# Kernel tuning notes

Hardware: AMD Instinct MI355X
Metric: run time of the kernel (lower is better)

Reference implementation:

```python
import jax, jax.numpy as jnp
import numpy as np

N_NODES = 50000
E_DIM = 128
H_DIM = 256
OUT_DIM = 2
N_EDGES = 800000
NEG_SLOPE = 0.01  # nn.LeakyReLU default


def gcn_conv(x, W, b, src, dst, n):
    """PyG GCNConv: h = x @ W; add self-loops; sym-normalized scatter-add; + bias."""
    h = x @ W  # [N, H]
    loop = jnp.arange(n, dtype=src.dtype)
    s = jnp.concatenate([src, loop])
    d = jnp.concatenate([dst, loop])
    w = jnp.ones_like(s, dtype=h.dtype)
    deg = jax.ops.segment_sum(w, d, num_segments=n)  # in-degree incl. self-loop
    dis = jnp.where(deg > 0, jax.lax.rsqrt(deg), jnp.zeros_like(deg))
    norm = dis[s] * dis[d]  # [E+N]
    msg = h[s] * norm[:, None]  # gather + scale
    out = jax.ops.segment_sum(msg, d, num_segments=n)  # scatter-add to targets
    return out + b


def setup_inputs() -> dict:
    key = jax.random.key(0)
    ks = jax.random.split(key, 12)
    inp = {
        "mask_feature": jax.random.normal(ks[0], (N_NODES, E_DIM), jnp.float32),
        "feature": jax.random.normal(ks[1], (N_NODES, E_DIM), jnp.float32),
        "edge_index": jax.random.randint(ks[2], (2, N_EDGES), 0, N_NODES, jnp.int64 if jax.config.jax_enable_x64 else jnp.int32),
        "edge_type": jax.random.randint(ks[3], (N_EDGES,), 0, 2, jnp.int64 if jax.config.jax_enable_x64 else jnp.int32),
        # learned parameters
        "W_in": jax.random.normal(ks[4], (E_DIM, H_DIM), jnp.float32) * 0.05,
        "b_in": jnp.zeros((H_DIM,), jnp.float32),
        "Wg1": jax.random.normal(ks[5], (H_DIM, H_DIM), jnp.float32) * 0.05,
        "bg1": jnp.zeros((H_DIM,), jnp.float32),
        "Wg2": jax.random.normal(ks[6], (H_DIM, H_DIM), jnp.float32) * 0.05,
        "bg2": jnp.zeros((H_DIM,), jnp.float32),
        "W_out": jax.random.normal(ks[7], (H_DIM, OUT_DIM), jnp.float32) * 0.05,
        "b_out": jnp.zeros((OUT_DIM,), jnp.float32),
    }
    return inp


def reference(mask_feature, feature, edge_index, edge_type,
              W_in, b_in, Wg1, bg1, Wg2, bg2, W_out, b_out):
    src, dst = edge_index[0], edge_index[1]
    n = mask_feature.shape[0]
    # main branch
    x = jax.nn.leaky_relu(mask_feature @ W_in + b_in, NEG_SLOPE)
    x = gcn_conv(x, Wg1, bg1, src, dst, n)
    # dropout is identity at inference
    x = gcn_conv(x, Wg2, bg2, src, dst, n)
    x = x @ W_out + b_out  # [N, out_dim]
    # mask branch
    m = jax.nn.leaky_relu((feature - mask_feature) @ W_in + b_in, NEG_SLOPE)
    m = m @ W_out + b_out  # [N, out_dim]
    return x * m
```

## Files before the change

### kernel.cpp

```cpp
#include <hip/hip_runtime.h>


#define NEG_SLOPE 0.01f
constexpr int HD = 256;
constexpr int CHUNK = 4096;
constexpr int BSTRIDE = 8192;

typedef __bf16 bf16x8 __attribute__((ext_vector_type(8)));
typedef unsigned short u16x8 __attribute__((ext_vector_type(8)));
typedef float f32x4 __attribute__((ext_vector_type(4)));

#define MFMA16 __builtin_amdgcn_mfma_f32_16x16x32_bf16

__device__ inline void split1(float v, unsigned short& h, unsigned short& l) {
  unsigned u = __float_as_uint(v);
  unsigned hb = u & 0xFFFF0000u;
  float lf = v - __uint_as_float(hb);
  unsigned ul = __float_as_uint(lf);
  h = (unsigned short)(hb >> 16);
  l = (unsigned short)((ul + 0x7FFFu + ((ul >> 16) & 1u)) >> 16);
}

__global__ __launch_bounds__(256) void k_prep(
    const float* __restrict__ Win, u16x8* __restrict__ Wf,
    const float* __restrict__ Wg1, const float* __restrict__ Wg2,
    const float* __restrict__ Wo, const float* __restrict__ bg1,
    const float* __restrict__ bg2, const float* __restrict__ bo,
    float* __restrict__ wb, float* __restrict__ uv, int* __restrict__ cur) {
  __shared__ float wt[256][2];
  const int bid = blockIdx.x, tid = threadIdx.x;
  if (bid < 32) {
    int f = bid * 4 + (tid >> 6);
    int lane = tid & 63;
    int nt = f >> 3, ks = (f >> 1) & 3, hl = f & 1;
    int n = nt * 16 + (lane & 15);
    int k0 = ks * 32 + (lane >> 4) * 8;
    u16x8 outv;
    #pragma unroll
    for (int j = 0; j < 8; ++j) {
      unsigned short h, l;
      split1(Win[(size_t)(k0 + j) * HD + n], h, l);
      outv[j] = hl ? l : h;
    }
    Wf[f * 64 + lane] = outv;
  } else if (bid == 32) {
    int r = tid;
    float s0 = 0.f, s1 = 0.f;
    for (int k = 0; k < 256; ++k) {
      float w = Wg2[r * 256 + k];
      s0 = fmaf(w, Wo[k * 2 + 0], s0);
      s1 = fmaf(w, Wo[k * 2 + 1], s1);
    }
    wt[r][0] = s0; wt[r][1] = s1;
    __syncthreads();
    float b0 = 0.f, b1 = 0.f;
    for (int k = 0; k < 256; ++k) {
      float w = Wg1[r * 256 + k];
      b0 = fmaf(w, wt[k][0], b0);
      b1 = fmaf(w, wt[k][1], b1);
    }
    wb[r * 2 + 0] = b0; wb[r * 2 + 1] = b1;
    if (r < 2) {
      float u = 0.f, v = 0.f;
      for (int k = 0; k < 256; ++k) {
        u = fmaf(bg1[k], wt[k][r], u);
        v = fmaf(bg2[k], Wo[k * 2 + r], v);
      }
      uv[r] = u;
      uv[2 + r] = v + bo[r];
    }
  } else {
    cur[tid] = 0;
  }
}

__global__ __launch_bounds__(256) void k_scatter(
    const int* __restrict__ src, const int* __restrict__ dst,
    int* __restrict__ cur, unsigned* __restrict__ packed, int E) {
  __shared__ int bins[256], lstart[256], gbase[256], lcur[256];
  __shared__ int wsum[4];
  __shared__ unsigned sbuf[CHUNK];
  const int t = threadIdx.x, b = blockIdx.x;
  const int lane = t & 63, wid = t >> 6;
  bins[t] = 0;
  __syncthreads();
  const int e0 = b * CHUNK, e1 = min(e0 + CHUNK, E), m = e1 - e0;
  for (int e = e0 + t; e < e1; e += 256)
    atomicAdd(&bins[dst[e] >> 8], 1);
  __syncthreads();
  {
    int v = bins[t], incl = v;
    #pragma unroll
    for (int o = 1; o < 64; o <<= 1) {
      int tmp = __shfl_up(incl, o, 64);
      if (lane >= o) incl += tmp;
    }
    if (lane == 63) wsum[wid] = incl;
    __syncthreads();
    int woff = 0;
    for (int w = 0; w < wid; ++w) woff += wsum[w];
    int st = woff + incl - v;
    lstart[t] = st;
    lcur[t] = st;
    gbase[t] = v ? atomicAdd(&cur[t], v) : 0;
  }
  __syncthreads();
  for (int e = e0 + t; e < e1; e += 256) {
    int d = dst[e], s = src[e];
    int slot = atomicAdd(&lcur[d >> 8], 1);
    sbuf[slot] = ((unsigned)d << 16) | (unsigned)s;
  }
  __syncthreads();
  for (int i = t; i < m; i += 256) {
    unsigned pv = sbuf[i];
    int bin = pv >> 24;
    packed[(size_t)bin * BSTRIDE + gbase[bin] + (i - lstart[bin])] = pv;
  }
}

__global__ __launch_bounds__(256, 2) void k_main(
    const float* __restrict__ mf, const float* __restrict__ fe,
    const u16x8* __restrict__ Wf, const float* __restrict__ bi,
    const float* __restrict__ wb, const float* __restrict__ Wo,
    const float* __restrict__ bo, float4* __restrict__ q, float* __restrict__ Pm,
    const unsigned* __restrict__ packed, const int* __restrict__ cur,
    int* __restrict__ rp, int* __restrict__ csr, int N, int Gg) {
  __shared__ __align__(16) char smem[18560];
  const int tid = threadIdx.x;
  const int lane = tid & 63, wid = tid >> 6;

  if ((int)blockIdx.x < Gg) {
    float4* sE1 = (float4*)smem;
    float2* sE2 = (float2*)(smem + 4096);
    sE1[tid] = make_float4(bi[tid], wb[2 * tid], wb[2 * tid + 1], 0.f);
    sE2[tid] = make_float2(Wo[2 * tid], Wo[2 * tid + 1]);

    const int gb = blockIdx.x * 64;
    const int base = gb + wid * 16;
    int arow = base + (lane & 15);
    if (arow >= N) arow = N - 1;
    const int kb = (lane >> 4) * 8;
    const float* ap = mf + (size_t)arow * 128 + kb;
    const float* fp = fe + (size_t)arow * 128 + kb;

    bf16x8 Ah[4], Al[4], Kh[4], Kl[4];
    #pragma unroll
    for (int ks = 0; ks < 4; ++ks) {
      float x[8], y[8];
      *(float4*)&x[0] = *(const float4*)(ap + ks * 32);
      *(float4*)&x[4] = *(const float4*)(ap + ks * 32 + 4);
      *(float4*)&y[0] = *(const float4*)(fp + ks * 32);
      *(float4*)&y[4] = *(const float4*)(fp + ks * 32 + 4);
      u16x8 hA, lA, hM, lM;
      #pragma unroll
      for (int j = 0; j < 8; ++j) {
        unsigned short hh, ll;
        split1(x[j], hh, ll);        hA[j] = hh; lA[j] = ll;
        split1(y[j] - x[j], hh, ll); hM[j] = hh; lM[j] = ll;
      }
      Ah[ks] = __builtin_bit_cast(bf16x8, hA);
      Al[ks] = __builtin_bit_cast(bf16x8, lA);
      Kh[ks] = __builtin_bit_cast(bf16x8, hM);
      Kl[ks] = __builtin_bit_cast(bf16x8, lM);
    }
    __syncthreads();

    const u16x8* wp = Wf + lane;
    float s0[4] = {}, s1[4] = {}, t0v[4] = {}, t1v[4] = {};
    u16x8 bA[8], bB[8];
    #pragma unroll
    for (int f = 0; f < 8; ++f) bA[f] = wp[f * 64];

    auto COMPUTE = [&](const u16x8* b, int nt) {
      f32x4 a0 = {0,0,0,0}, a1 = {0,0,0,0}, a2 = {0,0,0,0};
      f32x4 k0 = {0,0,0,0}, k1 = {0,0,0,0}, k2 = {0,0,0,0};
      #pragma unroll
      for (int ks = 0; ks < 4; ++ks) {
        bf16x8 bh = __builtin_bit_cast(bf16x8, b[ks * 2 + 0]);
        bf16x8 bl = __builtin_bit_cast(bf16x8, b[ks * 2 + 1]);
        a0 = MFMA16(Ah[ks], bh, a0, 0, 0, 0);
        a1 = MFMA16(Al[ks], bh, a1, 0, 0, 0);
        a2 = MFMA16(Ah[ks], bl, a2, 0, 0, 0);
        k0 = MFMA16(Kh[ks], bh, k0, 0, 0, 0);
        k1 = MFMA16(Kl[ks], bh, k1, 0, 0, 0);
        k2 = MFMA16(Kh[ks], bl, k2, 0, 0, 0);
      }
      const int col = nt * 16 + (lane & 15);
      const float4 e1 = sE1[col];
      const float2 e2 = sE2[col];
      #pragma unroll
      for (int r = 0; r < 4; ++r) {
        float a = (a0[r] + a1[r]) + (a2[r] + e1.x);
        a = a > 0.f ? a : NEG_SLOPE * a;
        s0[r] = fmaf(a, e1.y, s0[r]); s1[r] = fmaf(a, e1.z, s1[r]);
        float m = (k0[r] + k1[r]) + (k2[r] + e1.x);
        m = m > 0.f ? m : NEG_SLOPE * m;
        t0v[r] = fmaf(m, e2.x, t0v[r]); t1v[r] = fmaf(m, e2.y, t1v[r]);
      }
    };

    #pragma unroll 1
    for (int nt = 0; nt < 16; nt += 2) {
      #pragma unroll
      for (int f = 0; f < 8; ++f) bB[f] = wp[((nt + 1) * 8 + f) * 64];
      COMPUTE(bA, nt);
      if (nt + 2 < 16) {
        #pragma unroll
        for (int f = 0; f < 8; ++f) bA[f] = wp[((nt + 2) * 8 + f) * 64];
      }
      COMPUTE(bB, nt + 1);
    }

    #pragma unroll
    for (int o = 1; o < 16; o <<= 1) {
      #pragma unroll
      for (int r = 0; r < 4; ++r) {
        s0[r] += __shfl_xor(s0[r], o, 16);  s1[r] += __shfl_xor(s1[r], o, 16);
        t0v[r] += __shfl_xor(t0v[r], o, 16); t1v[r] += __shfl_xor(t1v[r], o, 16);
      }
    }
    if ((lane & 15) == 0) {
      float bo0 = bo[0], bo1 = bo[1];
      #pragma unroll
      for (int r = 0; r < 4; ++r) {
        int row = base + (lane >> 4) * 4 + r;
        if (row < N) {
          float* qf = (float*)&q[row];
          qf[1] = s0[r];
          qf[2] = s1[r];
          Pm[row * 2 + 0] = t0v[r] + bo0;
          Pm[row * 2 + 1] = t1v[r] + bo1;
        }
      }
    }
    return;
  }

  int* cnt = (int*)smem;
  int* sc  = (int*)(smem + 1024);
  int* wsum = (int*)(smem + 2048);
  unsigned short* sbuf = (unsigned short*)(smem + 2064);
  const int t = tid;
  const int B = blockIdx.x - Gg;
  int tot = cur[t], incl = tot;
  #pragma unroll
  for (int o = 1; o < 64; o <<= 1) {
    int tmp = __shfl_up(incl, o, 64);
    if (lane >= o) incl += tmp;
  }
  if (lane == 63) wsum[wid] = incl;
  __syncthreads();
  int woff = 0;
  for (int w = 0; w < wid; ++w) woff += wsum[w];
  sc[t] = woff + incl - tot;
  __syncthreads();
  const int base = sc[B];
  const int ecnt = cur[B];
  const unsigned* pk = packed + (size_t)B * BSTRIDE;
  cnt[t] = 0;
  __syncthreads();
  for (int i = t; i < ecnt; i += 256)
    atomicAdd(&cnt[(pk[i] >> 16) & 0xFF], 1);
  __syncthreads();
  int v = cnt[t];
  incl = v;
  #pragma unroll
  for (int o = 1; o < 64; o <<= 1) {
    int tmp = __shfl_up(incl, o, 64);
    if (lane >= o) incl += tmp;
  }
  if (lane == 63) wsum[wid] = incl;
  __syncthreads();
  woff = 0;
  for (int w = 0; w < wid; ++w) woff += wsum[w];
  const int off = woff + incl - v;
  const int node = B * 256 + t;
  if (node < N) {
    rp[node] = base + off;
    ((float*)&q[node])[0] = rsqrtf((float)(v + 1));
  } else if (node == N) {
    rp[N] = base + off;
  }
  __syncthreads();
  cnt[t] = off;
  __syncthreads();
  for (int i = t; i < ecnt; i += 256) {
    unsigned pv = pk[i];
    int slot = atomicAdd(&cnt[(pv >> 16) & 0xFF], 1);
    sbuf[slot] = (unsigned short)(pv & 0xFFFFu);
  }
  __syncthreads();
  for (int i = t; i < ecnt; i += 256)
    csr[base + i] = (int)sbuf[i];
}

__global__ __launch_bounds__(256) void k_gather1(
    const int* __restrict__ rp, const int* __restrict__ csr,
    const float4* __restrict__ q, const float* __restrict__ uv,
    float* __restrict__ T2, int N) {
  int t = threadIdx.x;
  int n = blockIdx.x * 64 + (t >> 2);
  int l = t & 3;
  if (n >= N) return;
  int s0 = rp[n], s1 = rp[n + 1];
  float a0 = 0.f, a1 = 0.f;
  int j = s0 + l;
  for (; j + 12 < s1; j += 16) {
    int i0 = csr[j], i1 = csr[j + 4], i2 = csr[j + 8], i3 = csr[j + 12];
    float4 q0 = q[i0], q1 = q[i1], q2 = q[i2], q3 = q[i3];
    a0 = fmaf(q0.x, q0.y, a0); a1 = fmaf(q0.x, q0.z, a1);
    a0 = fmaf(q1.x, q1.y, a0); a1 = fmaf(q1.x, q1.z, a1);
    a0 = fmaf(q2.x, q2.y, a0); a1 = fmaf(q2.x, q2.z, a1);
    a0 = fmaf(q3.x, q3.y, a0); a1 = fmaf(q3.x, q3.z, a1);
  }
  for (; j < s1; j += 4) {
    float4 qa = q[csr[j]];
    a0 = fmaf(qa.x, qa.y, a0); a1 = fmaf(qa.x, qa.z, a1);
  }
  a0 += __shfl_xor(a0, 1, 4); a1 += __shfl_xor(a1, 1, 4);
  a0 += __shfl_xor(a0, 2, 4); a1 += __shfl_xor(a1, 2, 4);
  if (l == 0) {
    float4 qn = q[n];
    float d = qn.x;
    T2[n * 2 + 0] = d * (d * fmaf(d, qn.y, a0) + uv[0]);
    T2[n * 2 + 1] = d * (d * fmaf(d, qn.z, a1) + uv[1]);
  }
}

__global__ __launch_bounds__(256) void k_gather2(
    const int* __restrict__ rp, const int* __restrict__ csr,
    const float* __restrict__ T2, const float4* __restrict__ q,
    const float* __restrict__ uv, const float* __restrict__ Pm,
    float* __restrict__ out, int N) {
  int t = threadIdx.x;
  int n = blockIdx.x * 64 + (t >> 2);
  int l = t & 3;
  if (n >= N) return;
  int s0 = rp[n], s1 = rp[n + 1];
  float a0 = 0.f, a1 = 0.f;
  int j = s0 + l;
  for (; j + 12 < s1; j += 16) {
    int i0 = csr[j], i1 = csr[j + 4], i2 = csr[j + 8], i3 = csr[j + 12];
    float2 v0 = *(const float2*)&T2[i0 * 2];
    float2 v1 = *(const float2*)&T2[i1 * 2];
    float2 v2 = *(const float2*)&T2[i2 * 2];
    float2 v3 = *(const float2*)&T2[i3 * 2];
    a0 += (v0.x + v1.x) + (v2.x + v3.x);
    a1 += (v0.y + v1.y) + (v2.y + v3.y);
  }
  for (; j < s1; j += 4) {
    float2 va = *(const float2*)&T2[csr[j] * 2];
    a0 += va.x; a1 += va.y;
  }
  a0 += __shfl_xor(a0, 1, 4); a1 += __shfl_xor(a1, 1, 4);
  a0 += __shfl_xor(a0, 2, 4); a1 += __shfl_xor(a1, 2, 4);
  if (l == 0) {
    float d = q[n].x;
    float2 tv = *(const float2*)&T2[n * 2];
    float z0 = d * (tv.x + a0) + uv[2];
    float z1 = d * (tv.y + a1) + uv[3];
    out[n * 2 + 0] = z0 * Pm[n * 2 + 0];
    out[n * 2 + 1] = z1 * Pm[n * 2 + 1];
  }
}

extern "C" void kernel_launch(void* const* d_in, const int* in_sizes, int n_in,
                              void* d_out, int out_size, void* d_ws, size_t ws_size,
                              hipStream_t stream) {
  const float* mf  = (const float*)d_in[0];
  const float* fe  = (const float*)d_in[1];
  const int*   ei  = (const int*)d_in[2];
  const float* Win = (const float*)d_in[4];
  const float* bin = (const float*)d_in[5];
  const float* Wg1 = (const float*)d_in[6];
  const float* bg1 = (const float*)d_in[7];
  const float* Wg2 = (const float*)d_in[8];
  const float* bg2 = (const float*)d_in[9];
  const float* Wo  = (const float*)d_in[10];
  const float* bo  = (const float*)d_in[11];
  float* out = (float*)d_out;

  const int ED = 128;
  const int N = in_sizes[0] / ED;
  const int E = in_sizes[3];
  const int* src = ei;
  const int* dst = ei + E;

  char* ws = (char*)d_ws;
  size_t off = 0;
  auto carve = [&](size_t bytes) {
    char* p = ws + off;
    off += (bytes + 255) & ~(size_t)255;
    return p;
  };
  int*      cur    = (int*)carve(256 * 4);
  unsigned* packed = (unsigned*)carve((size_t)256 * BSTRIDE * 4);
  int*      csr    = (int*)carve((size_t)E * 4);
  int*      rp     = (int*)carve((size_t)(N + 1) * 4);
  float4*   q      = (float4*)carve((size_t)N * 16);
  float*    T2     = (float*)carve((size_t)N * 2 * 4);
  float*    Pm     = (float*)carve((size_t)N * 2 * 4);
  float*    wb     = (float*)carve((size_t)HD * 2 * 4);
  float*    uv     = (float*)carve(4 * 4);
  u16x8*    Wf     = (u16x8*)carve((size_t)128 * 64 * 16);
  (void)ws_size; (void)n_in; (void)out_size;

  const int NB  = (E + CHUNK - 1) / CHUNK;
  const int NP2 = (N + 255) / 256;
  const int Gg  = (N + 63) / 64;
  const int Gt  = (N + 63) / 64;

  k_prep<<<34, 256, 0, stream>>>(Win, Wf, Wg1, Wg2, Wo, bg1, bg2, bo, wb, uv, cur);
  k_scatter<<<NB, 256, 0, stream>>>(src, dst, cur, packed, E);
  k_main<<<Gg + NP2, 256, 0, stream>>>(mf, fe, Wf, bin, wb, Wo, bo, q, Pm,
                                       packed, cur, rp, csr, N, Gg);
  k_gather1<<<Gt, 256, 0, stream>>>(rp, csr, q, uv, T2, N);
  k_gather2<<<Gt, 256, 0, stream>>>(rp, csr, T2, q, uv, Pm, out, N);
}
```

Before: 92.58 us.

## Drop low-half weight split in MFMA GEMM and widen gather to 8 lanes per node

The W_in weights are now rounded to a single bf16 instead of a hi/lo split, so the main GEMM issues four MFMAs per k-step instead of six. It also halves the weight-fragment loads and register buffers. Separately, the two CSR gather kernels now use 8 lanes per node with 2-way unrolling instead of 4 lanes with 4-way unrolling, for more parallelism per node. The weight change lowers accuracy of the input projection, since weight rounding error is no longer compensated.

```diff
diff --git a/kernel.cpp b/kernel.cpp
--- a/kernel.cpp
+++ b/kernel.cpp
@@ -19,6 +19,11 @@
   unsigned ul = __float_as_uint(lf);
   h = (unsigned short)(hb >> 16);
   l = (unsigned short)((ul + 0x7FFFu + ((ul >> 16) & 1u)) >> 16);
+}
+
+__device__ inline unsigned short bf16rne(float v) {
+  unsigned u = __float_as_uint(v);
+  return (unsigned short)((u + 0x7FFFu + ((u >> 16) & 1u)) >> 16);
 }
 
 __global__ __launch_bounds__(256) void k_prep(
@@ -29,21 +34,18 @@
     float* __restrict__ wb, float* __restrict__ uv, int* __restrict__ cur) {
   __shared__ float wt[256][2];
   const int bid = blockIdx.x, tid = threadIdx.x;
-  if (bid < 32) {
+  if (bid < 16) {
     int f = bid * 4 + (tid >> 6);
     int lane = tid & 63;
-    int nt = f >> 3, ks = (f >> 1) & 3, hl = f & 1;
+    int nt = f >> 2, ks = f & 3;
     int n = nt * 16 + (lane & 15);
     int k0 = ks * 32 + (lane >> 4) * 8;
     u16x8 outv;
     #pragma unroll
-    for (int j = 0; j < 8; ++j) {
-      unsigned short h, l;
-      split1(Win[(size_t)(k0 + j) * HD + n], h, l);
-      outv[j] = hl ? l : h;
-    }
+    for (int j = 0; j < 8; ++j)
+      outv[j] = bf16rne(Win[(size_t)(k0 + j) * HD + n]);
     Wf[f * 64 + lane] = outv;
-  } else if (bid == 32) {
+  } else if (bid == 16) {
     int r = tid;
     float s0 = 0.f, s1 = 0.f;
     for (int k = 0; k < 256; ++k) {
@@ -167,33 +169,30 @@
 
     const u16x8* wp = Wf + lane;
     float s0[4] = {}, s1[4] = {}, t0v[4] = {}, t1v[4] = {};
-    u16x8 bA[8], bB[8];
+    u16x8 bA[4], bB[4];
     #pragma unroll
-    for (int f = 0; f < 8; ++f) bA[f] = wp[f * 64];
+    for (int f = 0; f < 4; ++f) bA[f] = wp[f * 64];
 
     auto COMPUTE = [&](const u16x8* b, int nt) {
-      f32x4 a0 = {0,0,0,0}, a1 = {0,0,0,0}, a2 = {0,0,0,0};
-      f32x4 k0 = {0,0,0,0}, k1 = {0,0,0,0}, k2 = {0,0,0,0};
+      f32x4 a0 = {0,0,0,0}, a1 = {0,0,0,0};
+      f32x4 k0 = {0,0,0,0}, k1 = {0,0,0,0};
       #pragma unroll
       for (int ks = 0; ks < 4; ++ks) {
-        bf16x8 bh = __builtin_bit_cast(bf16x8, b[ks * 2 + 0]);
-        bf16x8 bl = __builtin_bit_cast(bf16x8, b[ks * 2 + 1]);
+        bf16x8 bh = __builtin_bit_cast(bf16x8, b[ks]);
         a0 = MFMA16(Ah[ks], bh, a0, 0, 0, 0);
         a1 = MFMA16(Al[ks], bh, a1, 0, 0, 0);
-        a2 = MFMA16(Ah[ks], bl, a2, 0, 0, 0);
         k0 = MFMA16(Kh[ks], bh, k0, 0, 0, 0);
         k1 = MFMA16(Kl[ks], bh, k1, 0, 0, 0);
-        k2 = MFMA16(Kh[ks], bl, k2, 0, 0, 0);
       }
       const int col = nt * 16 + (lane & 15);
       const float4 e1 = sE1[col];
       const float2 e2 = sE2[col];
       #pragma unroll
       for (int r = 0; r < 4; ++r) {
-        float a = (a0[r] + a1[r]) + (a2[r] + e1.x);
+        float a = (a0[r] + a1[r]) + e1.x;
         a = a > 0.f ? a : NEG_SLOPE * a;
         s0[r] = fmaf(a, e1.y, s0[r]); s1[r] = fmaf(a, e1.z, s1[r]);
-        float m = (k0[r] + k1[r]) + (k2[r] + e1.x);
+        float m = (k0[r] + k1[r]) + e1.x;
         m = m > 0.f ? m : NEG_SLOPE * m;
         t0v[r] = fmaf(m, e2.x, t0v[r]); t1v[r] = fmaf(m, e2.y, t1v[r]);
       }
@@ -202,11 +201,11 @@
     #pragma unroll 1
     for (int nt = 0; nt < 16; nt += 2) {
       #pragma unroll
-      for (int f = 0; f < 8; ++f) bB[f] = wp[((nt + 1) * 8 + f) * 64];
+      for (int f = 0; f < 4; ++f) bB[f] = wp[((nt + 1) * 4 + f) * 64];
       COMPUTE(bA, nt);
       if (nt + 2 < 16) {
         #pragma unroll
-        for (int f = 0; f < 8; ++f) bA[f] = wp[((nt + 2) * 8 + f) * 64];
+        for (int f = 0; f < 4; ++f) bA[f] = wp[((nt + 2) * 4 + f) * 64];
       }
       COMPUTE(bB, nt + 1);
     }
@@ -299,26 +298,25 @@
     const float4* __restrict__ q, const float* __restrict__ uv,
     float* __restrict__ T2, int N) {
   int t = threadIdx.x;
-  int n = blockIdx.x * 64 + (t >> 2);
-  int l = t & 3;
+  int n = blockIdx.x * 32 + (t >> 3);
+  int l = t & 7;
   if (n >= N) return;
   int s0 = rp[n], s1 = rp[n + 1];
   float a0 = 0.f, a1 = 0.f;
   int j = s0 + l;
-  for (; j + 12 < s1; j += 16) {
-    int i0 = csr[j], i1 = csr[j + 4], i2 = csr[j + 8], i3 = csr[j + 12];
-    float4 q0 = q[i0], q1 = q[i1], q2 = q[i2], q3 = q[i3];
+  for (; j + 8 < s1; j += 16) {
+    int i0 = csr[j], i1 = csr[j + 8];
+    float4 q0 = q[i0], q1 = q[i1];
     a0 = fmaf(q0.x, q0.y, a0); a1 = fmaf(q0.x, q0.z, a1);
     a0 = fmaf(q1.x, q1.y, a0); a1 = fmaf(q1.x, q1.z, a1);
-    a0 = fmaf(q2.x, q2.y, a0); a1 = fmaf(q2.x, q2.z, a1);
-    a0 = fmaf(q3.x, q3.y, a0); a1 = fmaf(q3.x, q3.z, a1);
-  }
-  for (; j < s1; j += 4) {
+  }
+  if (j < s1) {
     float4 qa = q[csr[j]];
     a0 = fmaf(qa.x, qa.y, a0); a1 = fmaf(qa.x, qa.z, a1);
   }
-  a0 += __shfl_xor(a0, 1, 4); a1 += __shfl_xor(a1, 1, 4);
-  a0 += __shfl_xor(a0, 2, 4); a1 += __shfl_xor(a1, 2, 4);
+  a0 += __shfl_xor(a0, 1, 8); a1 += __shfl_xor(a1, 1, 8);
+  a0 += __shfl_xor(a0, 2, 8); a1 += __shfl_xor(a1, 2, 8);
+  a0 += __shfl_xor(a0, 4, 8); a1 += __shfl_xor(a1, 4, 8);
   if (l == 0) {
     float4 qn = q[n];
     float d = qn.x;
@@ -333,27 +331,25 @@
     const float* __restrict__ uv, const float* __restrict__ Pm,
     float* __restrict__ out, int N) {
   int t = threadIdx.x;
-  int n = blockIdx.x * 64 + (t >> 2);
-  int l = t & 3;
+  int n = blockIdx.x * 32 + (t >> 3);
+  int l = t & 7;
   if (n >= N) return;
   int s0 = rp[n], s1 = rp[n + 1];
   float a0 = 0.f, a1 = 0.f;
   int j = s0 + l;
-  for (; j + 12 < s1; j += 16) {
-    int i0 = csr[j], i1 = csr[j + 4], i2 = csr[j + 8], i3 = csr[j + 12];
+  for (; j + 8 < s1; j += 16) {
+    int i0 = csr[j], i1 = csr[j + 8];
     float2 v0 = *(const float2*)&T2[i0 * 2];
     float2 v1 = *(const float2*)&T2[i1 * 2];
-    float2 v2 = *(const float2*)&T2[i2 * 2];
-    float2 v3 = *(const float2*)&T2[i3 * 2];
-    a0 += (v0.x + v1.x) + (v2.x + v3.x);
-    a1 += (v0.y + v1.y) + (v2.y + v3.y);
-  }
-  for (; j < s1; j += 4) {
+    a0 += v0.x + v1.x; a1 += v0.y + v1.y;
+  }
+  if (j < s1) {
     float2 va = *(const float2*)&T2[csr[j] * 2];
     a0 += va.x; a1 += va.y;
   }
-  a0 += __shfl_xor(a0, 1, 4); a1 += __shfl_xor(a1, 1, 4);
-  a0 += __shfl_xor(a0, 2, 4); a1 += __shfl_xor(a1, 2, 4);
+  a0 += __shfl_xor(a0, 1, 8); a1 += __shfl_xor(a1, 1, 8);
+  a0 += __shfl_xor(a0, 2, 8); a1 += __shfl_xor(a1, 2, 8);
+  a0 += __shfl_xor(a0, 4, 8); a1 += __shfl_xor(a1, 4, 8);
   if (l == 0) {
     float d = q[n].x;
     float2 tv = *(const float2*)&T2[n * 2];
@@ -402,15 +398,15 @@
   float*    Pm     = (float*)carve((size_t)N * 2 * 4);
   float*    wb     = (float*)carve((size_t)HD * 2 * 4);
   float*    uv     = (float*)carve(4 * 4);
-  u16x8*    Wf     = (u16x8*)carve((size_t)128 * 64 * 16);
+  u16x8*    Wf     = (u16x8*)carve((size_t)64 * 64 * 16);
   (void)ws_size; (void)n_in; (void)out_size;
 
   const int NB  = (E + CHUNK - 1) / CHUNK;
   const int NP2 = (N + 255) / 256;
   const int Gg  = (N + 63) / 64;
-  const int Gt  = (N + 63) / 64;
-
-  k_prep<<<34, 256, 0, stream>>>(Win, Wf, Wg1, Wg2, Wo, bg1, bg2, bo, wb, uv, cur);
+  const int Gt  = (N + 31) / 32;
+
+  k_prep<<<18, 256, 0, stream>>>(Win, Wf, Wg1, Wg2, Wo, bg1, bg2, bo, wb, uv, cur);
   k_scatter<<<NB, 256, 0, stream>>>(src, dst, cur, packed, E);
   k_main<<<Gg + NP2, 256, 0, stream>>>(mf, fe, Wf, bin, wb, Wo, bo, q, Pm,
                                        packed, cur, rp, csr, N, Gg);
```

Measured after the change: 84.11 us. -9.1%, faster.
